# Performance work log

Measured on AMD Instinct MI355X. Metric: run time of the kernel, lower is better.

Reference implementation:

```python
import jax, jax.numpy as jnp
import numpy as np

B, LVS, WIDTH, DEPTH = 8192, 512, 512, 7
EPS = 1e-5
SLOPE = 0.01  # torch LeakyReLU default negative_slope


def setup_inputs() -> dict:
    key = jax.random.key(0)
    ks = jax.random.split(key, 16)
    inp = {"x": jax.random.normal(ks[0], (B, LVS), dtype=jnp.float32)}
    for i in range(DEPTH):
        fan_in = LVS + WIDTH * i
        inp[f"W{i}"] = jax.random.normal(ks[1 + i], (WIDTH, fan_in), dtype=jnp.float32) / np.sqrt(fan_in)
    inp["b"] = 0.01 * jax.random.normal(ks[8], (DEPTH, WIDTH), dtype=jnp.float32)
    inp["gamma"] = jnp.ones((DEPTH, WIDTH), dtype=jnp.float32)
    inp["beta"] = jnp.zeros((DEPTH, WIDTH), dtype=jnp.float32)
    cin = LVS + DEPTH * WIDTH  # 4096
    inp["Wc"] = jax.random.normal(ks[9], (1, cin), dtype=jnp.float32) / np.sqrt(cin)
    inp["bc"] = jnp.zeros((1,), dtype=jnp.float32)
    # torch: rv = randn(...) * 0.02 + 1, multiplied onto each projection
    inp["noise"] = 1.0 + 0.02 * jax.random.normal(ks[10], (DEPTH, B, WIDTH), dtype=jnp.float32)
    return inp


def reference(x, W0, W1, W2, W3, W4, W5, W6, b, gamma, beta, Wc, bc, noise):
    Ws = (W0, W1, W2, W3, W4, W5, W6)
    last = x
    for i in range(DEPTH):
        # Linear: [B, in_i] @ [in_i, width]
        h = jnp.einsum('bi,wi->bw', last, Ws[i]) + b[i]
        # BatchNorm1d (training mode: batch stats, biased variance)
        mean = jnp.mean(h, axis=0)
        var = jnp.mean(jnp.square(h - mean), axis=0)
        h = (h - mean) * jax.lax.rsqrt(var + EPS) * gamma[i] + beta[i]
        # LeakyReLU + multiplicative noise, fused elementwise
        h = jnp.where(h >= 0, h, SLOPE * h) * noise[i]
        last = jnp.concatenate((last, h), axis=-1)
    logits = jnp.einsum('bi,oi->bo', last, Wc) + bc
    return jax.nn.sigmoid(logits)
```

## Files before the change

### kernel.cpp

```cpp
#include <hip/hip_runtime.h>

#define B_ROWS 8192
#define WIDTH  512
#define DEPTH  7
#define CIN    4096
#define EPS    1e-5f
#define SLOPE  0.01f

typedef __attribute__((ext_vector_type(8))) short short8;
typedef __attribute__((ext_vector_type(4))) short short4v;
typedef __attribute__((ext_vector_type(4))) float f32x4;

__device__ inline short f2bf(float f) {
  unsigned u = __builtin_bit_cast(unsigned, f);
  unsigned r = (u + 0x7FFFu + ((u >> 16) & 1u)) >> 16;
  return (short)r;
}

__device__ inline void gl_lds16(const void* g, void* l) {
  __builtin_amdgcn_global_load_lds(
      (const __attribute__((address_space(1))) unsigned*)g,
      (__attribute__((address_space(3))) unsigned*)l, 16, 0, 0);
}

struct WP { const float* p[7]; };

__global__ __launch_bounds__(256) void convw(WP wp, short* __restrict__ out) {
  long e = ((long)blockIdx.x * 256 + threadIdx.x) * 4;
  int layer; long base;
  if      (e < 262144L)  { layer = 0; base = 0; }
  else if (e < 786432L)  { layer = 1; base = 262144L; }
  else if (e < 1572864L) { layer = 2; base = 786432L; }
  else if (e < 2621440L) { layer = 3; base = 1572864L; }
  else if (e < 3932160L) { layer = 4; base = 2621440L; }
  else if (e < 5505024L) { layer = 5; base = 3932160L; }
  else                   { layer = 6; base = 5505024L; }
  f32x4 v = *(const f32x4*)(wp.p[layer] + (e - base));
  short4v o;
  o.x = f2bf(v.x); o.y = f2bf(v.y); o.z = f2bf(v.z); o.w = f2bf(v.w);
  *(short4v*)(out + e) = o;
}

__global__ __launch_bounds__(256) void initx(const float* __restrict__ x,
                                             const float* __restrict__ wc,
                                             short* __restrict__ lastbf,
                                             float* __restrict__ logit) {
  int w = threadIdx.x >> 6, l = threadIdx.x & 63;
  int r = blockIdx.x * 4 + w;
  const float* xr = x + (long)r * 512 + l * 8;
  f32x4 v0 = *(const f32x4*)xr;
  f32x4 v1 = *(const f32x4*)(xr + 4);
  const float* wcr = wc + l * 8;
  float acc = 0.f;
  short8 ob;
#pragma unroll
  for (int j = 0; j < 4; ++j) { acc += v0[j] * wcr[j];     ob[j]     = f2bf(v0[j]); }
#pragma unroll
  for (int j = 0; j < 4; ++j) { acc += v1[j] * wcr[4 + j]; ob[4 + j] = f2bf(v1[j]); }
  *(short8*)&lastbf[(long)r * CIN + l * 8] = ob;
#pragma unroll
  for (int off = 32; off; off >>= 1) acc += __shfl_xor(acc, off);
  if (l == 0) logit[r] = acc;
}

__global__ __launch_bounds__(512, 4) void gemm_fused(const short* __restrict__ A,
                                                     const short* __restrict__ Bw,
                                                     float* __restrict__ C,
                                                     float* __restrict__ sums,
                                                     int K) {
  __shared__ __align__(16) char smem[49152];
  int t = threadIdx.x;
  int w = t >> 6, l = t & 63;
  int ks = w >> 2, wq = w & 3;
  int wm = wq >> 1, wn = wq & 1;
  int lr = l & 15;
  int lg = l >> 4;
  int kb = ks * 64 + lg * 16;

  int bm = blockIdx.x, bn = blockIdx.y;
  const short* Ab = A + (long)(bm * 64) * CIN;
  const short* Bb = Bw + (long)(bn * 128) * K;

  f32x4 acc[2][4];
#pragma unroll
  for (int m = 0; m < 2; ++m)
#pragma unroll
    for (int n = 0; n < 4; ++n) acc[m][n] = f32x4{0.f, 0.f, 0.f, 0.f};

  int l8 = l >> 3;
  int scol = ((l & 7) ^ l8) << 3;

#define STAGE(buf, k0)                                                          \
  {                                                                             \
    char* base = smem + (buf) * 24576;                                          \
    gl_lds16(Ab + (long)(w * 8 + l8) * CIN + (k0) + scol,      base + w * 1024);\
    gl_lds16(Bb + (long)(w * 8 + l8) * K + (k0) + scol,        base + 8192 + w * 1024); \
    gl_lds16(Bb + (long)(64 + w * 8 + l8) * K + (k0) + scol,   base + 16384 + w * 1024);\
  }

  STAGE(0, 0);
  __syncthreads();

  int nt = K >> 6;
  int cur = 0;
  for (int tix = 0; tix < nt; ++tix) {
    if (tix + 1 < nt) STAGE(cur ^ 1, (tix + 1) << 6);
    const char* AsC = smem + cur * 24576;
    const char* BsC = AsC + 8192;
    short8 a[2], b[4];
#pragma unroll
    for (int m = 0; m < 2; ++m) {
      int row = wm * 32 + m * 16 + lr;
      a[m] = *(const short8*)(AsC + ((row * 128 + kb) ^ ((lr & 7) << 4)));
    }
#pragma unroll
    for (int n = 0; n < 4; ++n) {
      int row = wn * 64 + n * 16 + lr;
      b[n] = *(const short8*)(BsC + ((row * 128 + kb) ^ ((lr & 7) << 4)));
    }
#pragma unroll
    for (int m = 0; m < 2; ++m)
#pragma unroll
      for (int n = 0; n < 4; ++n)
        acc[m][n] = __builtin_amdgcn_mfma_f32_16x16x32_bf16(a[m], b[n], acc[m][n], 0, 0, 0);
    __syncthreads();
    cur ^= 1;
  }

  float* Red = (float*)smem;
  if (ks == 1) {
#pragma unroll
    for (int m = 0; m < 2; ++m)
#pragma unroll
      for (int n = 0; n < 4; ++n)
#pragma unroll
        for (int j = 0; j < 4; ++j)
          Red[wq * 2048 + (m * 16 + lg * 4 + j) * 64 + n * 16 + lr] = acc[m][n][j];
  }
  __syncthreads();
  if (ks == 0) {
    float* Cb = C + (long)(bm * 64 + wm * 32) * WIDTH + bn * 128 + wn * 64;
#pragma unroll
    for (int n = 0; n < 4; ++n) {
      float s = 0.f, q = 0.f;
#pragma unroll
      for (int m = 0; m < 2; ++m) {
#pragma unroll
        for (int j = 0; j < 4; ++j) {
          float v = acc[m][n][j] + Red[wq * 2048 + (m * 16 + lg * 4 + j) * 64 + n * 16 + lr];
          Cb[(long)(m * 16 + lg * 4 + j) * WIDTH + n * 16 + lr] = v;
          s += v; q += v * v;
        }
      }
      s += __shfl_xor(s, 16); s += __shfl_xor(s, 32);
      q += __shfl_xor(q, 16); q += __shfl_xor(q, 32);
      if (l < 16) {
        int colg = bn * 128 + wn * 64 + n * 16 + l;
        atomicAdd(&sums[colg], s);
        atomicAdd(&sums[WIDTH + colg], q);
      }
    }
  }
#undef STAGE
}

__global__ __launch_bounds__(256) void bnact(const float* __restrict__ h,
                                             const float* __restrict__ sums,
                                             const float* __restrict__ gamma,
                                             const float* __restrict__ beta,
                                             const float* __restrict__ noise,
                                             const float* __restrict__ wc,
                                             short* __restrict__ lastseg,
                                             float* __restrict__ logit) {
  int w = threadIdx.x >> 6, l = threadIdx.x & 63;
  int r = blockIdx.x * 4 + w;
  int c = l * 8;
  const float invB = 1.0f / 8192.0f;
  f32x4 h0 = *(const f32x4*)&h[(long)r * WIDTH + c];
  f32x4 h1 = *(const f32x4*)&h[(long)r * WIDTH + c + 4];
  f32x4 n0 = *(const f32x4*)&noise[(long)r * WIDTH + c];
  f32x4 n1 = *(const f32x4*)&noise[(long)r * WIDTH + c + 4];
  float acc = 0.f;
  short8 ob;
#pragma unroll
  for (int j = 0; j < 8; ++j) {
    int cc = c + j;
    float hv = j < 4 ? h0[j] : h1[j - 4];
    float nv = j < 4 ? n0[j] : n1[j - 4];
    float mean = sums[cc] * invB;
    float var = sums[WIDTH + cc] * invB - mean * mean;
    float v = (hv - mean) * rsqrtf(var + EPS);
    v = v * gamma[cc] + beta[cc];
    v = v >= 0.f ? v : SLOPE * v;
    v *= nv;
    acc += v * wc[cc];
    ob[j] = f2bf(v);
  }
  *(short8*)&lastseg[(long)r * CIN + c] = ob;
#pragma unroll
  for (int off = 32; off; off >>= 1) acc += __shfl_xor(acc, off);
  if (l == 0) logit[r] += acc;
}

__global__ __launch_bounds__(256) void finalize(const float* __restrict__ logit,
                                                const float* __restrict__ bc,
                                                float* __restrict__ out) {
  int i = blockIdx.x * 256 + threadIdx.x;
  float z = logit[i] + bc[0];
  out[i] = 1.0f / (1.0f + expf(-z));
}

extern "C" void kernel_launch(void* const* d_in, const int* in_sizes, int n_in,
                              void* d_out, int out_size, void* d_ws, size_t ws_size,
                              hipStream_t stream) {
  (void)in_sizes; (void)n_in; (void)out_size; (void)ws_size;
  const float* x     = (const float*)d_in[0];
  WP wp;
  for (int i = 0; i < 7; ++i) wp.p[i] = (const float*)d_in[1 + i];
  const float* gamma = (const float*)d_in[9];
  const float* beta  = (const float*)d_in[10];
  const float* Wc    = (const float*)d_in[11];
  const float* bc    = (const float*)d_in[12];
  const float* noise = (const float*)d_in[13];

  char* ws = (char*)d_ws;
  short* lastbf = (short*)ws;
  float* hpre   = (float*)(ws + 67108864);
  short* wbf    = (short*)(ws + 67108864 + 16777216);
  float* sums   = (float*)(ws + 67108864 + 16777216 + 14680064);
  float* logit  = (float*)(ws + 67108864 + 16777216 + 14680064 + 28672);

  hipMemsetAsync(sums, 0, DEPTH * 1024 * sizeof(float), stream);
  convw<<<7168, 256, 0, stream>>>(wp, wbf);
  initx<<<2048, 256, 0, stream>>>(x, Wc, lastbf, logit);

  long woff = 0;
  for (int i = 0; i < DEPTH; ++i) {
    int K = 512 * (i + 1);
    gemm_fused<<<dim3(128, 4), 512, 0, stream>>>(lastbf, wbf + woff, hpre,
                                                 sums + i * 1024, K);
    bnact<<<2048, 256, 0, stream>>>(hpre, sums + i * 1024,
                                    gamma + i * 512, beta + i * 512,
                                    noise + (long)i * B_ROWS * WIDTH,
                                    Wc + 512 + i * 512,
                                    lastbf + 512 + (long)i * 512, logit);
    woff += (long)512 * K;
  }
  finalize<<<32, 256, 0, stream>>>(logit, bc, (float*)d_out);
}
```

Before: 310.6 us.

## Switch GEMM to 32x32x16 MFMA with 4-way split-K over 256-thread blocks

```diff
diff --git a/kernel.cpp b/kernel.cpp
--- a/kernel.cpp
+++ b/kernel.cpp
@@ -10,6 +10,7 @@
 typedef __attribute__((ext_vector_type(8))) short short8;
 typedef __attribute__((ext_vector_type(4))) short short4v;
 typedef __attribute__((ext_vector_type(4))) float f32x4;
+typedef __attribute__((ext_vector_type(16))) float f32x16;
 
 __device__ inline short f2bf(float f) {
   unsigned u = __builtin_bit_cast(unsigned, f);
@@ -44,7 +45,10 @@
 __global__ __launch_bounds__(256) void initx(const float* __restrict__ x,
                                              const float* __restrict__ wc,
                                              short* __restrict__ lastbf,
-                                             float* __restrict__ logit) {
+                                             float* __restrict__ logit,
+                                             float* __restrict__ sumsz) {
+  int gid = blockIdx.x * 256 + threadIdx.x;
+  if (gid < DEPTH * 1024) sumsz[gid] = 0.f;
   int w = threadIdx.x >> 6, l = threadIdx.x & 63;
   int r = blockIdx.x * 4 + w;
   const float* xr = x + (long)r * 512 + l * 8;
@@ -63,104 +67,124 @@
   if (l == 0) logit[r] = acc;
 }
 
-__global__ __launch_bounds__(512, 4) void gemm_fused(const short* __restrict__ A,
+__global__ __launch_bounds__(256, 2) void gemm_fused(const short* __restrict__ A,
                                                      const short* __restrict__ Bw,
                                                      float* __restrict__ C,
                                                      float* __restrict__ sums,
                                                      int K) {
   __shared__ __align__(16) char smem[49152];
   int t = threadIdx.x;
-  int w = t >> 6, l = t & 63;
-  int ks = w >> 2, wq = w & 3;
-  int wm = wq >> 1, wn = wq & 1;
-  int lr = l & 15;
-  int lg = l >> 4;
-  int kb = ks * 64 + lg * 16;
-
+  int ks = t >> 6, l = t & 63;
+  int l31 = l & 31, hi = l >> 5;
   int bm = blockIdx.x, bn = blockIdx.y;
-  const short* Ab = A + (long)(bm * 64) * CIN;
-  const short* Bb = Bw + (long)(bn * 128) * K;
-
-  f32x4 acc[2][4];
-#pragma unroll
-  for (int m = 0; m < 2; ++m)
-#pragma unroll
-    for (int n = 0; n < 4; ++n) acc[m][n] = f32x4{0.f, 0.f, 0.f, 0.f};
+  const short* Ab = A + (long)(bm * 128) * CIN;
+  const short* Bb = Bw + (long)(bn * 64) * K;
+
+  f32x16 acc[4][2];
+#pragma unroll
+  for (int m = 0; m < 4; ++m)
+#pragma unroll
+    for (int n = 0; n < 2; ++n)
+#pragma unroll
+      for (int r = 0; r < 16; ++r) acc[m][n][r] = 0.f;
 
   int l8 = l >> 3;
   int scol = ((l & 7) ^ l8) << 3;
 
-#define STAGE(buf, k0)                                                          \
-  {                                                                             \
-    char* base = smem + (buf) * 24576;                                          \
-    gl_lds16(Ab + (long)(w * 8 + l8) * CIN + (k0) + scol,      base + w * 1024);\
-    gl_lds16(Bb + (long)(w * 8 + l8) * K + (k0) + scol,        base + 8192 + w * 1024); \
-    gl_lds16(Bb + (long)(64 + w * 8 + l8) * K + (k0) + scol,   base + 16384 + w * 1024);\
+#define STAGE(buf, k0)                                                                       \
+  {                                                                                          \
+    char* base = smem + (buf) * 24576;                                                       \
+    int c0 = ks * 4, c1 = ks * 2;                                                            \
+    gl_lds16(Ab + (long)((c0    ) * 8 + l8) * CIN + (k0) + scol, base + (c0    ) * 1024);    \
+    gl_lds16(Ab + (long)((c0 + 1) * 8 + l8) * CIN + (k0) + scol, base + (c0 + 1) * 1024);    \
+    gl_lds16(Ab + (long)((c0 + 2) * 8 + l8) * CIN + (k0) + scol, base + (c0 + 2) * 1024);    \
+    gl_lds16(Ab + (long)((c0 + 3) * 8 + l8) * CIN + (k0) + scol, base + (c0 + 3) * 1024);    \
+    gl_lds16(Bb + (long)((c1    ) * 8 + l8) * K + (k0) + scol, base + 16384 + (c1    ) * 1024); \
+    gl_lds16(Bb + (long)((c1 + 1) * 8 + l8) * K + (k0) + scol, base + 16384 + (c1 + 1) * 1024); \
   }
 
   STAGE(0, 0);
   __syncthreads();
+
+  int kb = ks * 32 + hi * 16;
+  int sw = (l & 7) << 4;
 
   int nt = K >> 6;
   int cur = 0;
   for (int tix = 0; tix < nt; ++tix) {
     if (tix + 1 < nt) STAGE(cur ^ 1, (tix + 1) << 6);
     const char* AsC = smem + cur * 24576;
-    const char* BsC = AsC + 8192;
-    short8 a[2], b[4];
-#pragma unroll
-    for (int m = 0; m < 2; ++m) {
-      int row = wm * 32 + m * 16 + lr;
-      a[m] = *(const short8*)(AsC + ((row * 128 + kb) ^ ((lr & 7) << 4)));
-    }
-#pragma unroll
-    for (int n = 0; n < 4; ++n) {
-      int row = wn * 64 + n * 16 + lr;
-      b[n] = *(const short8*)(BsC + ((row * 128 + kb) ^ ((lr & 7) << 4)));
-    }
-#pragma unroll
-    for (int m = 0; m < 2; ++m)
-#pragma unroll
-      for (int n = 0; n < 4; ++n)
-        acc[m][n] = __builtin_amdgcn_mfma_f32_16x16x32_bf16(a[m], b[n], acc[m][n], 0, 0, 0);
+    const char* BsC = AsC + 16384;
+    short8 a[4], b[2];
+#pragma unroll
+    for (int m = 0; m < 4; ++m)
+      a[m] = *(const short8*)(AsC + (m * 32 + l31) * 128 + (kb ^ sw));
+#pragma unroll
+    for (int n = 0; n < 2; ++n)
+      b[n] = *(const short8*)(BsC + (n * 32 + l31) * 128 + (kb ^ sw));
+#pragma unroll
+    for (int m = 0; m < 4; ++m)
+#pragma unroll
+      for (int n = 0; n < 2; ++n)
+        acc[m][n] = __builtin_amdgcn_mfma_f32_32x32x16_bf16(a[m], b[n], acc[m][n], 0, 0, 0);
     __syncthreads();
     cur ^= 1;
   }
 
   float* Red = (float*)smem;
+#define RIDX(m, n, r) (((m) * 32 + ((r) & 3) + 8 * ((r) >> 2) + 4 * hi) * 64 + (n) * 32 + l31)
+  if (ks == 3) {
+#pragma unroll
+    for (int m = 0; m < 4; ++m)
+#pragma unroll
+      for (int n = 0; n < 2; ++n)
+#pragma unroll
+        for (int r = 0; r < 16; ++r) Red[RIDX(m, n, r)] = acc[m][n][r];
+  }
+  __syncthreads();
+  if (ks == 2) {
+#pragma unroll
+    for (int m = 0; m < 4; ++m)
+#pragma unroll
+      for (int n = 0; n < 2; ++n)
+#pragma unroll
+        for (int r = 0; r < 16; ++r) Red[RIDX(m, n, r)] += acc[m][n][r];
+  }
+  __syncthreads();
   if (ks == 1) {
 #pragma unroll
-    for (int m = 0; m < 2; ++m)
-#pragma unroll
-      for (int n = 0; n < 4; ++n)
-#pragma unroll
-        for (int j = 0; j < 4; ++j)
-          Red[wq * 2048 + (m * 16 + lg * 4 + j) * 64 + n * 16 + lr] = acc[m][n][j];
+    for (int m = 0; m < 4; ++m)
+#pragma unroll
+      for (int n = 0; n < 2; ++n)
+#pragma unroll
+        for (int r = 0; r < 16; ++r) Red[RIDX(m, n, r)] += acc[m][n][r];
   }
   __syncthreads();
   if (ks == 0) {
-    float* Cb = C + (long)(bm * 64 + wm * 32) * WIDTH + bn * 128 + wn * 64;
-#pragma unroll
-    for (int n = 0; n < 4; ++n) {
+    float* Cb = C + (long)(bm * 128) * WIDTH + bn * 64;
+#pragma unroll
+    for (int n = 0; n < 2; ++n) {
       float s = 0.f, q = 0.f;
 #pragma unroll
-      for (int m = 0; m < 2; ++m) {
-#pragma unroll
-        for (int j = 0; j < 4; ++j) {
-          float v = acc[m][n][j] + Red[wq * 2048 + (m * 16 + lg * 4 + j) * 64 + n * 16 + lr];
-          Cb[(long)(m * 16 + lg * 4 + j) * WIDTH + n * 16 + lr] = v;
+      for (int m = 0; m < 4; ++m) {
+#pragma unroll
+        for (int r = 0; r < 16; ++r) {
+          int cr = (r & 3) + 8 * (r >> 2) + 4 * hi;
+          float v = acc[m][n][r] + Red[RIDX(m, n, r)];
+          Cb[(long)(m * 32 + cr) * WIDTH + n * 32 + l31] = v;
           s += v; q += v * v;
         }
       }
-      s += __shfl_xor(s, 16); s += __shfl_xor(s, 32);
-      q += __shfl_xor(q, 16); q += __shfl_xor(q, 32);
-      if (l < 16) {
-        int colg = bn * 128 + wn * 64 + n * 16 + l;
+      s += __shfl_xor(s, 32);
+      q += __shfl_xor(q, 32);
+      if (l < 32) {
+        int colg = bn * 64 + n * 32 + l;
         atomicAdd(&sums[colg], s);
         atomicAdd(&sums[WIDTH + colg], q);
       }
     }
   }
+#undef RIDX
 #undef STAGE
 }
 
@@ -230,15 +254,14 @@
   float* sums   = (float*)(ws + 67108864 + 16777216 + 14680064);
   float* logit  = (float*)(ws + 67108864 + 16777216 + 14680064 + 28672);
 
-  hipMemsetAsync(sums, 0, DEPTH * 1024 * sizeof(float), stream);
   convw<<<7168, 256, 0, stream>>>(wp, wbf);
-  initx<<<2048, 256, 0, stream>>>(x, Wc, lastbf, logit);
+  initx<<<2048, 256, 0, stream>>>(x, Wc, lastbf, logit, sums);
 
   long woff = 0;
   for (int i = 0; i < DEPTH; ++i) {
     int K = 512 * (i + 1);
-    gemm_fused<<<dim3(128, 4), 512, 0, stream>>>(lastbf, wbf + woff, hpre,
-                                                 sums + i * 1024, K);
+    gemm_fused<<<dim3(64, 8), 256, 0, stream>>>(lastbf, wbf + woff, hpre,
+                                                sums + i * 1024, K);
     bnact<<<2048, 256, 0, stream>>>(hpre, sums + i * 1024,
                                     gamma + i * 512, beta + i * 512,
                                     noise + (long)i * B_ROWS * WIDTH,
```

Result: faster. 287.9 us (-7.3%).
